# Kernel optimization log

Hardware: AMD Instinct MI355X
Metric: run time of the kernel (lower is better)

The kernel has to match this reference:

```python
import jax, jax.numpy as jnp
import numpy as np

N_ROLES = 6
EPS = 1e-5

def _ln(x, scale, bias):
    m = jnp.mean(x, axis=-1, keepdims=True)
    v = jnp.var(x, axis=-1, keepdims=True)
    return (x - m) * jax.lax.rsqrt(v + EPS) * scale + bias

def setup_inputs() -> dict:
    key = jax.random.key(0)
    ks = jax.random.split(key, 20)
    T, B, D_OBS, H, A = 32, 1024, 256, 512, 32
    inp = {
        'rnn_states': jax.random.normal(ks[0], (B, H), jnp.float32),
        'obs': jax.random.normal(ks[1], (T, B, D_OBS), jnp.float32),
        'resets': jnp.zeros((T, B), jnp.float32),
        'available_actions': jnp.ones((T, B, A), jnp.float32),
        'role_ids': jax.random.randint(ks[2], (T, B), 0, N_ROLES, jnp.int32),
        # feature norm over obs_dim
        'fn_scale': jnp.ones((D_OBS,), jnp.float32),
        'fn_bias': jnp.zeros((D_OBS,), jnp.float32),
        # base MLP: obs_dim->512->512, each followed by LayerNorm
        'W0': jax.random.normal(ks[3], (D_OBS, H), jnp.float32) * 0.02,
        'b0': jnp.zeros((H,), jnp.float32),
        'ln0_scale': jnp.ones((H,), jnp.float32),
        'ln0_bias': jnp.zeros((H,), jnp.float32),
        'W1': jax.random.normal(ks[4], (H, H), jnp.float32) * 0.02,
        'b1': jnp.zeros((H,), jnp.float32),
        'ln1_scale': jnp.ones((H,), jnp.float32),
        'ln1_bias': jnp.zeros((H,), jnp.float32),
        # per-role routes: obs_dim->128->H (stacked over roles)
        'Wr0': jax.random.normal(ks[5], (N_ROLES, D_OBS, 128), jnp.float32) * 0.02,
        'br0': jnp.zeros((N_ROLES, 128), jnp.float32),
        'Wr1': jax.random.normal(ks[6], (N_ROLES, 128, H), jnp.float32) * 0.02,
        'br1': jnp.zeros((N_ROLES, H), jnp.float32),
        # per-role heads: H->64->32->action_dim (stacked over roles)
        'Wh0': jax.random.normal(ks[7], (N_ROLES, H, 64), jnp.float32) * 0.02,
        'bh0': jnp.zeros((N_ROLES, 64), jnp.float32),
        'Wh1': jax.random.normal(ks[8], (N_ROLES, 64, 32), jnp.float32) * 0.02,
        'bh1': jnp.zeros((N_ROLES, 32), jnp.float32),
        'Wh2': jax.random.normal(ks[9], (N_ROLES, 32, A), jnp.float32) * 0.02,
        'bh2': jnp.zeros((N_ROLES, A), jnp.float32),
    }
    return inp

def _gather_by_role(all_values, role_ids):
    # all_values: (K, T, B, F); role_ids: (T, B) -> (T, B, F)
    idx = role_ids[None, :, :, None].astype(jnp.int32)
    return jnp.take_along_axis(all_values, idx, axis=0)[0]

def reference(rnn_states, obs, resets, available_actions, role_ids,
              fn_scale, fn_bias, W0, b0, ln0_scale, ln0_bias,
              W1, b1, ln1_scale, ln1_bias,
              Wr0, br0, Wr1, br1,
              Wh0, bh0, Wh1, bh1, Wh2, bh2):
    # feature normalization on raw obs
    obs_n = _ln(obs, fn_scale, fn_bias)
    # shared base MLP (relu + LayerNorm after each Dense)
    e = _ln(jax.nn.relu(obs_n @ W0 + b0), ln0_scale, ln0_bias)
    e = _ln(jax.nn.relu(e @ W1 + b1), ln1_scale, ln1_bias)
    # per-role pre-GRU residual routes on (normalized) obs
    r = jax.nn.relu(jnp.einsum('tbi,kih->ktbh', obs_n, Wr0) + br0[:, None, None, :])
    r = jax.nn.relu(jnp.einsum('ktbh,kho->ktbo', r, Wr1) + br1[:, None, None, :])
    e = e + _gather_by_role(r, role_ids)
    # no recurrent policy configured: rnn_states pass through
    # per-role heads -> all logits (K, T, B, A)
    h = jax.nn.relu(jnp.einsum('tbh,khf->ktbf', e, Wh0) + bh0[:, None, None, :])
    h = jax.nn.relu(jnp.einsum('ktbf,kfg->ktbg', h, Wh1) + bh1[:, None, None, :])
    all_logits = jnp.einsum('ktbg,kga->ktba', h, Wh2) + bh2[:, None, None, :]
    logits = _gather_by_role(all_logits, role_ids)
    logits = jnp.where(available_actions > 0.5, logits, jnp.full_like(logits, -1e10))
    return rnn_states, logits
```

## Files before the change

### kernel.cpp

```cpp
#include <hip/hip_runtime.h>
#include <stdint.h>

typedef unsigned short u16;
typedef unsigned int u32;

using bf16x8 = __attribute__((ext_vector_type(8))) short;
using f32x4  = __attribute__((ext_vector_type(4))) float;

#define DEVINL __device__ __forceinline__

DEVINL float b2f(u16 u) { return __builtin_bit_cast(float, (u32)u << 16); }
DEVINL u16 f2b(float f) {
  u32 u = __builtin_bit_cast(u32, f);
  u += 0x7FFFu + ((u >> 16) & 1u);
  return (u16)(u >> 16);
}

DEVINL void gll16(const u16* src, u16* dst) {
  __builtin_amdgcn_global_load_lds(
      (const __attribute__((address_space(1))) void*)(uintptr_t)src,
      (__attribute__((address_space(3))) void*)(uintptr_t)dst, 16, 0, 0);
}

#define MFMA __builtin_amdgcn_mfma_f32_16x16x32_bf16
#define NROLE 6

DEVINL void tp_tile(const float* __restrict__ s, u16* __restrict__ d,
                    int R, int C, int bx, int by, int z)
{
  __shared__ u16 tile[32][33];
  const size_t mstride = (size_t)R * C;
  s += (size_t)z * mstride;
  d += (size_t)z * mstride;
  int r0 = bx * 32, c0 = by * 32;
  int tx = threadIdx.x & 31, ty = threadIdx.x >> 5;
#pragma unroll
  for (int i = 0; i < 32; i += 8)
    tile[ty + i][tx] = f2b(s[(size_t)(r0 + ty + i) * C + (c0 + tx)]);
  __syncthreads();
#pragma unroll
  for (int i = 0; i < 32; i += 8)
    d[(size_t)(c0 + ty + i) * R + (r0 + tx)] = tile[tx][ty + i];
}

__global__ __launch_bounds__(256) void mega0(
    const float* W0, const float* W1, const float* Wr0, const float* Wr1, const float* Wh0,
    u16* W0t, u16* W1t, u16* Wr0t, u16* Wr1t, u16* Wh0t,
    const int* __restrict__ rid, int* __restrict__ blkCnt,
    const float* __restrict__ rnn, float* __restrict__ outRnn)
{
  int b = blockIdx.x;
  const int tid = threadIdx.x;
  if (b < 1152) {
    if (b < 128)      {            tp_tile(W0, W0t, 256, 512, b % 8,  b / 8, 0); }
    else if (b < 384) { b -= 128;  tp_tile(W1, W1t, 512, 512, b % 16, b / 16, 0); }
    else if (b < 576) { b -= 384;  int t = b / 8;  tp_tile(Wr0, Wr0t, 256, 128, b % 8,  t % 4,  t / 4); }
    else if (b < 960) { b -= 576;  int t = b / 4;  tp_tile(Wr1, Wr1t, 128, 512, b % 4,  t % 16, t / 16); }
    else              { b -= 960;  int t = b / 16; tp_tile(Wh0, Wh0t, 512, 64,  b % 16, t % 2,  t / 2); }
  } else if (b < 1280) {
    b -= 1152;
    __shared__ int h[NROLE];
    if (tid < NROLE) h[tid] = 0;
    __syncthreads();
    atomicAdd(&h[rid[b * 256 + tid]], 1);
    __syncthreads();
    if (tid < NROLE) blkCnt[b * NROLE + tid] = h[tid];
  } else {
    b -= 1280;
    const float4* src = (const float4*)rnn;
    float4* dst = (float4*)outRnn;
    int base = (b * 256 + tid) * 4;
#pragma unroll
    for (int i = 0; i < 4; ++i) dst[base + i] = src[base + i];
  }
}

__global__ __launch_bounds__(256, 2) void g0f(
    const float* __restrict__ obs, const float* __restrict__ fn_s,
    const float* __restrict__ fn_b, const u16* __restrict__ W0t,
    const float* __restrict__ b0, const float* __restrict__ ln0sc,
    const float* __restrict__ ln0bi, u16* __restrict__ obs_n,
    u16* __restrict__ C,
    const int* __restrict__ rid, const int* __restrict__ blkCnt,
    int* __restrict__ bucket, int* __restrict__ baseArr, int* __restrict__ cntArr)
{
  __shared__ __align__(16) u16 smem[20480];
  const int tid = threadIdx.x;

  if (blockIdx.x >= 512) {
    const int bx = blockIdx.x - 512;
    int* c = (int*)smem;
    int* preArr = c + 768;
    int* scnt   = c + 776;
    int* sbase  = c + 784;
    int* h      = c + 792;
    for (int i = tid; i < 128 * NROLE; i += 256) c[i] = blkCnt[i];
    if (tid < NROLE) h[tid] = 0;
    __syncthreads();
    if (tid < NROLE) {
      int k = tid, run = 0, pre = 0;
      for (int b = 0; b < 128; ++b) { if (b == bx) pre = run; run += c[b * NROLE + k]; }
      scnt[k] = run; preArr[k] = pre;
    }
    __syncthreads();
    if (tid == 0) {
      int r = 0;
      for (int k = 0; k < NROLE; ++k) { sbase[k] = r; r += scnt[k]; }
    }
    __syncthreads();
    if (bx == 0 && tid < NROLE) { baseArr[tid] = sbase[tid]; cntArr[tid] = scnt[tid]; }
    int i = bx * 256 + tid;
    int k = rid[i];
    int pos = atomicAdd(&h[k], 1);
    bucket[sbase[k] + preArr[k] + pos] = i;
    return;
  }

  u16* smA     = smem;
  float* redS  = (float*)&smem[16384];
  float* redSS = (float*)&smem[16896];
  float* prm   = (float*)&smem[17408];
  const int rowBase = blockIdx.x * 64;
  const int lane = tid & 63, wave = tid >> 6;
  const int quad = lane >> 4, lm = lane & 15, l7 = lm & 7;

#pragma unroll
  for (int i = tid; i < 512; i += 256) {
    prm[i] = b0[i]; prm[512 + i] = ln0sc[i]; prm[1024 + i] = ln0bi[i];
  }

  {
    const int r = tid >> 2, q = tid & 3;
    const float* xr = obs + (size_t)(rowBase + r) * 256 + q * 64;
    float x[64];
#pragma unroll
    for (int jj = 0; jj < 16; ++jj)
      *(float4*)&x[jj * 4] = *(const float4*)(xr + jj * 4);
    float s = 0.f, s2 = 0.f;
#pragma unroll
    for (int p = 0; p < 64; ++p) { s += x[p]; s2 += x[p] * x[p]; }
    s  += __shfl_xor(s, 1, 64);  s  += __shfl_xor(s, 2, 64);
    s2 += __shfl_xor(s2, 1, 64); s2 += __shfl_xor(s2, 2, 64);
    float m = s * (1.f / 256.f);
    float var = s2 * (1.f / 256.f) - m * m;
    float inv = rsqrtf(var + 1e-5f);
    const float* fs = fn_s + q * 64;
    const float* fb = fn_b + q * 64;
    u16* og = obs_n + (size_t)(rowBase + r) * 256 + q * 64;
#pragma unroll
    for (int j = 0; j < 8; ++j) {
      float4 fs0 = *(const float4*)(fs + j * 8);
      float4 fs1 = *(const float4*)(fs + j * 8 + 4);
      float4 fb0 = *(const float4*)(fb + j * 8);
      float4 fb1 = *(const float4*)(fb + j * 8 + 4);
      u16 yy[8] __attribute__((aligned(16)));
      yy[0] = f2b((x[j*8+0] - m) * inv * fs0.x + fb0.x);
      yy[1] = f2b((x[j*8+1] - m) * inv * fs0.y + fb0.y);
      yy[2] = f2b((x[j*8+2] - m) * inv * fs0.z + fb0.z);
      yy[3] = f2b((x[j*8+3] - m) * inv * fs0.w + fb0.w);
      yy[4] = f2b((x[j*8+4] - m) * inv * fs1.x + fb1.x);
      yy[5] = f2b((x[j*8+5] - m) * inv * fs1.y + fb1.y);
      yy[6] = f2b((x[j*8+6] - m) * inv * fs1.z + fb1.z);
      yy[7] = f2b((x[j*8+7] - m) * inv * fs1.w + fb1.w);
      int cch = q * 8 + j;
      *(uint4*)&smA[r * 256 + ((cch ^ (r & 7)) * 8)] = *(uint4*)yy;
      *(uint4*)(og + j * 8) = *(uint4*)yy;
    }
  }

  const int wn = wave * 128;
  u32 bOff[8];
#pragma unroll
  for (int j = 0; j < 8; ++j)
    bOff[j] = (u32)(wn + j * 16 + lm) * 256u + (u32)(quad * 8);
  f32x4 acc[4][8] = {};
  bf16x8 bR[2][8];
#pragma unroll
  for (int p = 0; p < 2; ++p)
#pragma unroll
    for (int j = 0; j < 8; ++j)
      bR[p][j] = *(const bf16x8*)(W0t + bOff[j] + p * 32);
  __syncthreads();

#pragma unroll
  for (int g = 0; g < 8; ++g) {
    bf16x8 cur[8];
#pragma unroll
    for (int j = 0; j < 8; ++j) cur[j] = bR[g & 1][j];
    if (g + 2 < 8) {
#pragma unroll
      for (int j = 0; j < 8; ++j)
        bR[g & 1][j] = *(const bf16x8*)(W0t + bOff[j] + (g + 2) * 32);
    }
    const int kc = g * 4;
    bf16x8 af[4];
#pragma unroll
    for (int i2 = 0; i2 < 4; ++i2)
      af[i2] = *(const bf16x8*)&smA[(i2 * 16 + lm) * 256 + (((quad + kc) ^ l7) * 8)];
#pragma unroll
    for (int i2 = 0; i2 < 4; ++i2)
#pragma unroll
      for (int j = 0; j < 8; ++j)
        acc[i2][j] = MFMA(af[i2], cur[j], acc[i2][j], 0, 0, 0);
  }

#pragma unroll
  for (int i2 = 0; i2 < 4; ++i2) {
#pragma unroll
    for (int r2 = 0; r2 < 4; ++r2) {
      float s = 0.f, ss = 0.f;
#pragma unroll
      for (int j = 0; j < 8; ++j) {
        float v = fmaxf(acc[i2][j][r2] + prm[wn + j * 16 + lm], 0.f);
        acc[i2][j][r2] = v;
        s += v; ss += v * v;
      }
#pragma unroll
      for (int o = 1; o < 16; o <<= 1) { s += __shfl_xor(s, o, 64); ss += __shfl_xor(ss, o, 64); }
      if (lm == 0) {
        int rowL = i2 * 16 + quad * 4 + r2;
        redS[rowL * 4 + wave] = s;
        redSS[rowL * 4 + wave] = ss;
      }
    }
  }
  __syncthreads();
#pragma unroll
  for (int i2 = 0; i2 < 4; ++i2) {
#pragma unroll
    for (int r2 = 0; r2 < 4; ++r2) {
      int rowL = i2 * 16 + quad * 4 + r2;
      float ts  = redS[rowL * 4 + 0] + redS[rowL * 4 + 1] + redS[rowL * 4 + 2] + redS[rowL * 4 + 3];
      float tss = redSS[rowL * 4 + 0] + redSS[rowL * 4 + 1] + redSS[rowL * 4 + 2] + redSS[rowL * 4 + 3];
      float m = ts * (1.f / 512.f);
      float var = tss * (1.f / 512.f) - m * m;
      float inv = rsqrtf(var + 1e-5f);
      size_t base = (size_t)(rowBase + rowL) * 512;
#pragma unroll
      for (int j = 0; j < 8; ++j) {
        int col = wn + j * 16 + lm;
        float y = (acc[i2][j][r2] - m) * inv * prm[512 + col] + prm[1024 + col];
        C[base + col] = f2b(y);
      }
    }
  }
}

template <int K>
__global__ __launch_bounds__(256, 2) void gemm_ln(
    const u16* __restrict__ A, const u16* __restrict__ Bt,
    const float* __restrict__ bias, const float* __restrict__ lnsc,
    const float* __restrict__ lnbi, u16* __restrict__ C)
{
  constexpr int BK = 128, NI = K / BK, NC = K / 32;
  __shared__ __align__(16) u16 As[2][64 * BK];
  __shared__ float redS[64][4];
  __shared__ float redSS[64][4];
  __shared__ float prm[1536];
  const int tid = threadIdx.x;
  const int rowBase = blockIdx.x * 64;
  const int lane = tid & 63, wave = tid >> 6;
#pragma unroll
  for (int i = tid; i < 512; i += 256) {
    prm[i] = bias[i]; prm[512 + i] = lnsc[i]; prm[1024 + i] = lnbi[i];
  }
  u32 aOff[4];
#pragma unroll
  for (int r = 0; r < 4; ++r) {
    int row = r * 16 + (tid >> 4);
    int chunk = tid & 15;
    aOff[r] = (u32)(rowBase + row) * (u32)K + (u32)((chunk ^ (row & 7)) * 8);
  }
  const int quad = lane >> 4, lm = lane & 15, l7 = lm & 7;
  const int wn = wave * 128;
  u32 bOff[8];
#pragma unroll
  for (int j = 0; j < 8; ++j)
    bOff[j] = (u32)(wn + j * 16 + lm) * (u32)K + (u32)(quad * 8);

  f32x4 acc[4][8] = {};

#pragma unroll
  for (int r = 0; r < 4; ++r)
    gll16(A + aOff[r], &As[0][r * 2048 + wave * 512]);
  bf16x8 bP[8];
#pragma unroll
  for (int j = 0; j < 8; ++j)
    bP[j] = *(const bf16x8*)(Bt + bOff[j]);
  __syncthreads();

  for (int i = 0; i < NI; ++i) {
    const u16* Ab = As[i & 1];
    if (i + 1 < NI) {
#pragma unroll
      for (int r = 0; r < 4; ++r)
        gll16(A + aOff[r] + (i + 1) * BK, &As[(i + 1) & 1][r * 2048 + wave * 512]);
    }
#pragma unroll
    for (int c = 0; c < 4; ++c) {
      const int g = i * 4 + c;
      bf16x8 bN[8];
      if (g + 1 < NC) {
#pragma unroll
        for (int j = 0; j < 8; ++j)
          bN[j] = *(const bf16x8*)(Bt + bOff[j] + (g + 1) * 32);
      }
      const int kc = c * 4;
      bf16x8 af[4];
#pragma unroll
      for (int i2 = 0; i2 < 4; ++i2)
        af[i2] = *(const bf16x8*)&Ab[(i2 * 16 + lm) * BK + (((quad + kc) ^ l7) * 8)];
#pragma unroll
      for (int i2 = 0; i2 < 4; ++i2)
#pragma unroll
        for (int j = 0; j < 8; ++j)
          acc[i2][j] = MFMA(af[i2], bP[j], acc[i2][j], 0, 0, 0);
      if (g + 1 < NC) {
#pragma unroll
        for (int j = 0; j < 8; ++j) bP[j] = bN[j];
      }
    }
    __syncthreads();
  }

#pragma unroll
  for (int i2 = 0; i2 < 4; ++i2) {
#pragma unroll
    for (int r2 = 0; r2 < 4; ++r2) {
      float s = 0.f, ss = 0.f;
#pragma unroll
      for (int j = 0; j < 8; ++j) {
        float v = fmaxf(acc[i2][j][r2] + prm[wn + j * 16 + lm], 0.f);
        acc[i2][j][r2] = v;
        s += v; ss += v * v;
      }
#pragma unroll
      for (int o = 1; o < 16; o <<= 1) { s += __shfl_xor(s, o, 64); ss += __shfl_xor(ss, o, 64); }
      if (lm == 0) {
        int rowL = i2 * 16 + quad * 4 + r2;
        redS[rowL][wave] = s;
        redSS[rowL][wave] = ss;
      }
    }
  }
  __syncthreads();
#pragma unroll
  for (int i2 = 0; i2 < 4; ++i2) {
#pragma unroll
    for (int r2 = 0; r2 < 4; ++r2) {
      int rowL = i2 * 16 + quad * 4 + r2;
      float ts  = redS[rowL][0] + redS[rowL][1] + redS[rowL][2] + redS[rowL][3];
      float tss = redSS[rowL][0] + redSS[rowL][1] + redSS[rowL][2] + redSS[rowL][3];
      float m = ts * (1.f / 512.f);
      float var = tss * (1.f / 512.f) - m * m;
      float inv = rsqrtf(var + 1e-5f);
      size_t base = (size_t)(rowBase + rowL) * 512;
#pragma unroll
      for (int j = 0; j < 8; ++j) {
        int col = wn + j * 16 + lm;
        float y = (acc[i2][j][r2] - m) * inv * prm[512 + col] + prm[1024 + col];
        C[base + col] = f2b(y);
      }
    }
  }
}

__global__ __launch_bounds__(256, 4) void route_head(
    const u16* __restrict__ obs_n, const u16* __restrict__ e,
    const u16* __restrict__ Wr0t, const float* __restrict__ br0,
    const u16* __restrict__ Wr1t, const float* __restrict__ br1,
    const u16* __restrict__ Wh0t, const float* __restrict__ bh0,
    const float* __restrict__ Wh1, const float* __restrict__ bh1,
    const float* __restrict__ Wh2, const float* __restrict__ bh2,
    const float* __restrict__ avail,
    const int* __restrict__ bucket, const int* __restrict__ baseArr,
    const int* __restrict__ cntArr, float* __restrict__ outLogits)
{
  __shared__ __align__(16) u16 sm[20480];
  const int tid = threadIdx.x;

  int cA0, cA1, cA2, cA3, cA4, cA5, bA0, bA1, bA2, bA3, bA4, bA5;
  {
    int4 ca = *(const int4*)cntArr;  int2 cb = *(const int2*)(cntArr + 4);
    int4 ba = *(const int4*)baseArr; int2 bb = *(const int2*)(baseArr + 4);
    cA0 = ca.x; cA1 = ca.y; cA2 = ca.z; cA3 = ca.w; cA4 = cb.x; cA5 = cb.y;
    bA0 = ba.x; bA1 = ba.y; bA2 = ba.z; bA3 = ba.w; bA4 = bb.x; bA5 = bb.y;
  }
  int role = -1, rem = blockIdx.x, cnt = 0, roleBase = 0;
#define TRY_ROLE(k, ck, bk)                                        \
  if (role < 0) {                                                  \
    int tiles = ((ck) + 31) >> 5;                                  \
    if (rem < tiles) { role = (k); cnt = (ck); roleBase = (bk); }  \
    else rem -= tiles;                                             \
  }
  TRY_ROLE(0, cA0, bA0) TRY_ROLE(1, cA1, bA1) TRY_ROLE(2, cA2, bA2)
  TRY_ROLE(3, cA3, bA3) TRY_ROLE(4, cA4, bA4) TRY_ROLE(5, cA5, bA5)
#undef TRY_ROLE
  if (role < 0) return;
  const int limit = cnt;
  const int rowBase = rem * 32;

  const int lane = tid & 63, wave = tid >> 6;
  const int quad = lane >> 4, lm = lane & 15, l7 = lm & 7;

#pragma unroll
  for (int r = 0; r < 8; ++r) {
    int lrow = r * 4 + wave;
    int i = rowBase + lrow;
    if (i >= limit) i = rowBase;
    int grow = bucket[roleBase + i];
    int chunk = tid & 63;
    int sw = (chunk & 56) | ((chunk ^ lrow) & 7);
    gll16(e + (u32)grow * 512u + (u32)(sw * 8), &sm[r * 2048 + wave * 512]);
  }

  int growA0, growA1;
  {
    int i0 = rowBase + lm;        if (i0 >= limit) i0 = rowBase;
    int i1 = rowBase + 16 + lm;   if (i1 >= limit) i1 = rowBase;
    growA0 = bucket[roleBase + i0];
    growA1 = bucket[roleBase + i1];
  }
  const u16* Ag0 = obs_n + (size_t)growA0 * 256;
  const u16* Ag1 = obs_n + (size_t)growA1 * 256;

  const int wn0 = wave * 32;
  const u16* B0 = Wr0t + (size_t)role * 128 * 256;
  f32x4 acc0[2][2] = {};
  bf16x8 b0R[2][2];
#pragma unroll
  for (int p = 0; p < 2; ++p)
#pragma unroll
    for (int j = 0; j < 2; ++j)
      b0R[p][j] = *(const bf16x8*)(B0 + (u32)(wn0 + j * 16 + lm) * 256u + (u32)(quad * 8 + p * 32));
  bf16x8 aR[4][2];
#pragma unroll
  for (int p = 0; p < 4; ++p) {
    aR[p][0] = *(const bf16x8*)(Ag0 + (u32)(quad * 8 + p * 32));
    aR[p][1] = *(const bf16x8*)(Ag1 + (u32)(quad * 8 + p * 32));
  }
  float bias0[2] = { br0[role * 128 + wn0 + lm], br0[role * 128 + wn0 + 16 + lm] };
#pragma unroll
  for (int it = 0; it < 8; ++it) {
    bf16x8 a0 = aR[it & 3][0], a1 = aR[it & 3][1];
    bf16x8 cur0 = b0R[it & 1][0], cur1 = b0R[it & 1][1];
    if (it + 2 < 8) {
#pragma unroll
      for (int j = 0; j < 2; ++j)
        b0R[it & 1][j] = *(const bf16x8*)(B0 + (u32)(wn0 + j * 16 + lm) * 256u + (u32)(quad * 8 + (it + 2) * 32));
    }
    if (it + 4 < 8) {
      aR[it & 3][0] = *(const bf16x8*)(Ag0 + (u32)(quad * 8 + (it + 4) * 32));
      aR[it & 3][1] = *(const bf16x8*)(Ag1 + (u32)(quad * 8 + (it + 4) * 32));
    }
    acc0[0][0] = MFMA(a0, cur0, acc0[0][0], 0, 0, 0);
    acc0[0][1] = MFMA(a0, cur1, acc0[0][1], 0, 0, 0);
    acc0[1][0] = MFMA(a1, cur0, acc0[1][0], 0, 0, 0);
    acc0[1][1] = MFMA(a1, cur1, acc0[1][1], 0, 0, 0);
  }
  u16* r1 = sm + 16384;
#pragma unroll
  for (int i2 = 0; i2 < 2; ++i2) {
#pragma unroll
    for (int r2 = 0; r2 < 4; ++r2) {
      int row = i2 * 16 + quad * 4 + r2;
#pragma unroll
      for (int j = 0; j < 2; ++j) {
        int col = wn0 + j * 16 + lm;
        float v = fmaxf(acc0[i2][j][r2] + bias0[j], 0.f);
        r1[row * 128 + (((col >> 3) ^ (row & 7)) * 8) + (col & 7)] = f2b(v);
      }
    }
  }
  __syncthreads();

  const int wn1 = wave * 128;
  const u16* B1 = Wr1t + (size_t)role * 512 * 128;
#pragma unroll
  for (int h = 0; h < 2; ++h) {
    const int wnh = wn1 + h * 64;
    float b1v[4];
#pragma unroll
    for (int j = 0; j < 4; ++j) b1v[j] = br1[role * 512 + wnh + j * 16 + lm];
    f32x4 acc1[2][4] = {};
    bf16x8 b1P[4];
#pragma unroll
    for (int j = 0; j < 4; ++j)
      b1P[j] = *(const bf16x8*)(B1 + (u32)(wnh + j * 16 + lm) * 128u + (u32)(quad * 8));
#pragma unroll
    for (int kk = 0; kk < 128; kk += 32) {
      bf16x8 b1N[4];
      if (kk + 32 < 128) {
#pragma unroll
        for (int j = 0; j < 4; ++j)
          b1N[j] = *(const bf16x8*)(B1 + (u32)(wnh + j * 16 + lm) * 128u + (u32)(quad * 8 + kk + 32));
      }
      const int kc = kk >> 3;
      bf16x8 af[2];
#pragma unroll
      for (int i2 = 0; i2 < 2; ++i2)
        af[i2] = *(const bf16x8*)&r1[(i2 * 16 + lm) * 128 + (((quad + kc) ^ l7) * 8)];
#pragma unroll
      for (int i2 = 0; i2 < 2; ++i2)
#pragma unroll
        for (int j = 0; j < 4; ++j)
          acc1[i2][j] = MFMA(af[i2], b1P[j], acc1[i2][j], 0, 0, 0);
      if (kk + 32 < 128) {
#pragma unroll
        for (int j = 0; j < 4; ++j) b1P[j] = b1N[j];
      }
    }
#pragma unroll
    for (int i2 = 0; i2 < 2; ++i2) {
#pragma unroll
      for (int r2 = 0; r2 < 4; ++r2) {
        int row = i2 * 16 + quad * 4 + r2;
#pragma unroll
        for (int j = 0; j < 4; ++j) {
          int col = wnh + j * 16 + lm;
          int addr = row * 512 + (((col >> 3) ^ (row & 7)) * 8) + (col & 7);
          float v = fmaxf(acc1[i2][j][r2] + b1v[j], 0.f) + b2f(sm[addr]);
          sm[addr] = f2b(v);
        }
      }
    }
  }
  __syncthreads();

  const int wn2 = wave * 16;
  const u16* B2 = Wh0t + (size_t)role * 64 * 512;
  float b2v = bh0[role * 64 + wn2 + lm];
  f32x4 acc2[2] = {};
  bf16x8 b2R[4];
#pragma unroll
  for (int p = 0; p < 4; ++p)
    b2R[p] = *(const bf16x8*)(B2 + (u32)(wn2 + lm) * 512u + (u32)(quad * 8 + p * 32));
#pragma unroll
  for (int it = 0; it < 16; ++it) {
    bf16x8 cur = b2R[it & 3];
    if (it + 4 < 16)
      b2R[it & 3] = *(const bf16x8*)(B2 + (u32)(wn2 + lm) * 512u + (u32)(quad * 8 + (it + 4) * 32));
    const int kc = it * 4;
    bf16x8 af[2];
#pragma unroll
    for (int i2 = 0; i2 < 2; ++i2)
      af[i2] = *(const bf16x8*)&sm[(i2 * 16 + lm) * 512 + (((quad + kc) ^ l7) * 8)];
#pragma unroll
    for (int i2 = 0; i2 < 2; ++i2)
      acc2[i2] = MFMA(af[i2], cur, acc2[i2], 0, 0, 0);
  }
  u16* h0s = sm + 16384;
#pragma unroll
  for (int i2 = 0; i2 < 2; ++i2) {
#pragma unroll
    for (int r2 = 0; r2 < 4; ++r2) {
      int row = i2 * 16 + quad * 4 + r2;
      int col = wn2 + lm;
      h0s[row * 68 + col] = f2b(fmaxf(acc2[i2][r2] + b2v, 0.f));
    }
  }
  __syncthreads();

  {
    float* h1s = (float*)&sm[16384];
    const int r = tid >> 3;
    const int n0 = (tid & 7) * 4;
    const bool valid = (rowBase + r) < limit;
    const float* W1k = Wh1 + (size_t)role * 64 * 32;
    const float* W2k = Wh2 + (size_t)role * 32 * 32;
    float4 a1 = *(const float4*)(bh1 + role * 32 + n0);
#pragma unroll 8
    for (int j = 0; j < 64; ++j) {
      float hj = b2f(h0s[r * 68 + j]);
      float4 wv = *(const float4*)(W1k + j * 32 + n0);
      a1.x += hj * wv.x; a1.y += hj * wv.y; a1.z += hj * wv.z; a1.w += hj * wv.w;
    }
    a1.x = fmaxf(a1.x, 0.f); a1.y = fmaxf(a1.y, 0.f);
    a1.z = fmaxf(a1.z, 0.f); a1.w = fmaxf(a1.w, 0.f);
    __syncthreads();
    h1s[r * 36 + n0 + 0] = a1.x;
    h1s[r * 36 + n0 + 1] = a1.y;
    h1s[r * 36 + n0 + 2] = a1.z;
    h1s[r * 36 + n0 + 3] = a1.w;
    __syncthreads();
    float4 a2 = *(const float4*)(bh2 + role * 32 + n0);
#pragma unroll 8
    for (int n = 0; n < 32; ++n) {
      float hn = h1s[r * 36 + n];
      float4 wv = *(const float4*)(W2k + n * 32 + n0);
      a2.x += hn * wv.x; a2.y += hn * wv.y; a2.z += hn * wv.z; a2.w += hn * wv.w;
    }
    if (valid) {
      int g = bucket[roleBase + rowBase + r];
      float4 av = *(const float4*)(avail + (size_t)g * 32 + n0);
      float4 o;
      o.x = (av.x > 0.5f) ? a2.x : -1e10f;
      o.y = (av.y > 0.5f) ? a2.y : -1e10f;
      o.z = (av.z > 0.5f) ? a2.z : -1e10f;
      o.w = (av.w > 0.5f) ? a2.w : -1e10f;
      *(float4*)(outLogits + (size_t)g * 32 + n0) = o;
    }
  }
}

extern "C" void kernel_launch(void* const* d_in, const int* in_sizes, int n_in,
                              void* d_out, int out_size, void* d_ws, size_t ws_size,
                              hipStream_t stream)
{
  const float* rnn  = (const float*)d_in[0];
  const float* obs  = (const float*)d_in[1];
  const float* avail= (const float*)d_in[3];
  const int*   rid  = (const int*)d_in[4];
  const float* fn_s = (const float*)d_in[5];
  const float* fn_b = (const float*)d_in[6];
  const float* W0   = (const float*)d_in[7];
  const float* b0   = (const float*)d_in[8];
  const float* ln0s = (const float*)d_in[9];
  const float* ln0b = (const float*)d_in[10];
  const float* W1   = (const float*)d_in[11];
  const float* b1   = (const float*)d_in[12];
  const float* ln1s = (const float*)d_in[13];
  const float* ln1b = (const float*)d_in[14];
  const float* Wr0  = (const float*)d_in[15];
  const float* br0  = (const float*)d_in[16];
  const float* Wr1  = (const float*)d_in[17];
  const float* br1  = (const float*)d_in[18];
  const float* Wh0  = (const float*)d_in[19];
  const float* bh0  = (const float*)d_in[20];
  const float* Wh1  = (const float*)d_in[21];
  const float* bh1  = (const float*)d_in[22];
  const float* Wh2  = (const float*)d_in[23];
  const float* bh2  = (const float*)d_in[24];

  const int ROWS = 32768;

  char* w = (char*)d_ws;
  auto carve = [&](size_t bytes) { char* p = w; w += (bytes + 255) & ~(size_t)255; return p; };
  u16* obs_n  = (u16*)carve((size_t)ROWS * 256 * 2);
  u16* bufA   = (u16*)carve((size_t)ROWS * 512 * 2);
  u16* bufB   = (u16*)carve((size_t)ROWS * 512 * 2);
  u16* W0t    = (u16*)carve((size_t)512 * 256 * 2);
  u16* W1t    = (u16*)carve((size_t)512 * 512 * 2);
  u16* Wr0t   = (u16*)carve((size_t)6 * 128 * 256 * 2);
  u16* Wr1t   = (u16*)carve((size_t)6 * 512 * 128 * 2);
  u16* Wh0t   = (u16*)carve((size_t)6 * 64 * 512 * 2);
  int* bucket = (int*)carve((size_t)ROWS * 4);
  int* blkCnt = (int*)carve((size_t)128 * NROLE * 4);
  int* baseArr= (int*)carve(256);
  int* cntArr = (int*)carve(256);

  float* outLogits = (float*)d_out + (size_t)1024 * 512;

  mega0<<<1408, 256, 0, stream>>>(W0, W1, Wr0, Wr1, Wh0, W0t, W1t, Wr0t, Wr1t, Wh0t,
                                  rid, blkCnt, rnn, (float*)d_out);

  g0f<<<640, 256, 0, stream>>>(obs, fn_s, fn_b, W0t, b0, ln0s, ln0b,
                               obs_n, bufA, rid, blkCnt, bucket, baseArr, cntArr);

  gemm_ln<512><<<512, 256, 0, stream>>>(bufA, W1t, b1, ln1s, ln1b, bufB);

  route_head<<<1029, 256, 0, stream>>>(obs_n, bufB, Wr0t, br0, Wr1t, br1, Wh0t, bh0,
                                       Wh1, bh1, Wh2, bh2, avail,
                                       bucket, baseArr, cntArr, outLogits);
}
```

Baseline: 271.1 us.

## Restructure route_head as single-wave blocks over 16-row tiles without barriers

The route/head kernel now runs one 64-thread wave per block on 16-row tiles instead of four waves on 32-row tiles, with 2053 blocks instead of 1029. Each wave computes every output column itself, which removes all __syncthreads and shrinks shared memory per block. The intent is more independent blocks, less barrier stalling and higher occupancy. The cost is that each wave reloads the full per-role weight tiles from global or cache with no software prefetch, and the tail MLP now handles 8 columns per lane.

```diff
diff --git a/kernel.cpp b/kernel.cpp
--- a/kernel.cpp
+++ b/kernel.cpp
@@ -365,7 +365,7 @@
   }
 }
 
-__global__ __launch_bounds__(256, 4) void route_head(
+__global__ __launch_bounds__(64, 2) void route_head(
     const u16* __restrict__ obs_n, const u16* __restrict__ e,
     const u16* __restrict__ Wr0t, const float* __restrict__ br0,
     const u16* __restrict__ Wr1t, const float* __restrict__ br1,
@@ -376,8 +376,8 @@
     const int* __restrict__ bucket, const int* __restrict__ baseArr,
     const int* __restrict__ cntArr, float* __restrict__ outLogits)
 {
-  __shared__ __align__(16) u16 sm[20480];
-  const int tid = threadIdx.x;
+  __shared__ __align__(16) u16 sm[11328];
+  const int lane = threadIdx.x;
 
   int cA0, cA1, cA2, cA3, cA4, cA5, bA0, bA1, bA2, bA3, bA4, bA5;
   {
@@ -389,7 +389,7 @@
   int role = -1, rem = blockIdx.x, cnt = 0, roleBase = 0;
 #define TRY_ROLE(k, ck, bk)                                        \
   if (role < 0) {                                                  \
-    int tiles = ((ck) + 31) >> 5;                                  \
+    int tiles = ((ck) + 15) >> 4;                                  \
     if (rem < tiles) { role = (k); cnt = (ck); roleBase = (bk); }  \
     else rem -= tiles;                                             \
   }
@@ -398,207 +398,148 @@
 #undef TRY_ROLE
   if (role < 0) return;
   const int limit = cnt;
-  const int rowBase = rem * 32;
-
-  const int lane = tid & 63, wave = tid >> 6;
-  const int quad = lane >> 4, lm = lane & 15, l7 = lm & 7;
-
-#pragma unroll
-  for (int r = 0; r < 8; ++r) {
-    int lrow = r * 4 + wave;
+  const int rowBase = rem * 16;
+
+  const int quad = lane >> 4, lm = lane & 15;
+
+#pragma unroll
+  for (int lrow = 0; lrow < 16; ++lrow) {
     int i = rowBase + lrow;
     if (i >= limit) i = rowBase;
     int grow = bucket[roleBase + i];
-    int chunk = tid & 63;
-    int sw = (chunk & 56) | ((chunk ^ lrow) & 7);
-    gll16(e + (u32)grow * 512u + (u32)(sw * 8), &sm[r * 2048 + wave * 512]);
-  }
-
-  int growA0, growA1;
+    int sw = (lane & 56) | ((lane ^ lrow) & 7);
+    gll16(e + (u32)grow * 512u + (u32)(sw * 8), &sm[lrow * 512]);
+  }
+
+  int iA = rowBase + lm; if (iA >= limit) iA = rowBase;
+  const u16* Ag = obs_n + (size_t)bucket[roleBase + iA] * 256 + quad * 8;
+
+  const u16* B0 = Wr0t + (size_t)role * 128 * 256;
+  f32x4 acc0[8] = {};
+#pragma unroll
+  for (int kc = 0; kc < 8; ++kc) {
+    bf16x8 a = *(const bf16x8*)(Ag + kc * 32);
+#pragma unroll
+    for (int j = 0; j < 8; ++j) {
+      bf16x8 b = *(const bf16x8*)(B0 + (u32)(j * 16 + lm) * 256u + (u32)(kc * 32 + quad * 8));
+      acc0[j] = MFMA(a, b, acc0[j], 0, 0, 0);
+    }
+  }
+  u16* r1 = sm + 8192;
+#pragma unroll
+  for (int j = 0; j < 8; ++j) {
+    float bv = br0[role * 128 + j * 16 + lm];
+#pragma unroll
+    for (int r2 = 0; r2 < 4; ++r2) {
+      int row = quad * 4 + r2;
+      int col = j * 16 + lm;
+      float v = fmaxf(acc0[j][r2] + bv, 0.f);
+      r1[row * 128 + (((col >> 3) ^ (row & 7)) * 8) + (col & 7)] = f2b(v);
+    }
+  }
+
+  const u16* B1 = Wr1t + (size_t)role * 512 * 128;
+#pragma unroll
+  for (int g = 0; g < 4; ++g) {
+    f32x4 acc1[8] = {};
+#pragma unroll
+    for (int kc = 0; kc < 4; ++kc) {
+      bf16x8 a = *(const bf16x8*)&r1[lm * 128 + (((kc * 4 + quad) ^ (lm & 7)) * 8)];
+#pragma unroll
+      for (int j = 0; j < 8; ++j) {
+        int col = g * 128 + j * 16 + lm;
+        bf16x8 b = *(const bf16x8*)(B1 + (u32)col * 128u + (u32)(kc * 32 + quad * 8));
+        acc1[j] = MFMA(a, b, acc1[j], 0, 0, 0);
+      }
+    }
+    if (g == 0) {
+      asm volatile("s_waitcnt vmcnt(0)" ::: "memory");
+      __builtin_amdgcn_sched_barrier(0);
+    }
+#pragma unroll
+    for (int j = 0; j < 8; ++j) {
+      int col = g * 128 + j * 16 + lm;
+      float bv = br1[role * 512 + col];
+#pragma unroll
+      for (int r2 = 0; r2 < 4; ++r2) {
+        int row = quad * 4 + r2;
+        int addr = row * 512 + (((col >> 3) ^ (row & 7)) * 8) + (col & 7);
+        float v = fmaxf(acc1[j][r2] + bv, 0.f) + b2f(sm[addr]);
+        sm[addr] = f2b(v);
+      }
+    }
+  }
+
+  const u16* B2 = Wh0t + (size_t)role * 64 * 512;
+  f32x4 acc2[4] = {};
+#pragma unroll
+  for (int kt = 0; kt < 16; ++kt) {
+    bf16x8 a = *(const bf16x8*)&sm[lm * 512 + (((kt * 4 + quad) ^ (lm & 7)) * 8)];
+#pragma unroll
+    for (int j = 0; j < 4; ++j) {
+      bf16x8 b = *(const bf16x8*)(B2 + (u32)(j * 16 + lm) * 512u + (u32)(kt * 32 + quad * 8));
+      acc2[j] = MFMA(a, b, acc2[j], 0, 0, 0);
+    }
+  }
+  u16* h0s = sm + 10240;
+#pragma unroll
+  for (int j = 0; j < 4; ++j) {
+    float bv = bh0[role * 64 + j * 16 + lm];
+#pragma unroll
+    for (int r2 = 0; r2 < 4; ++r2) {
+      int row = quad * 4 + r2;
+      h0s[row * 68 + j * 16 + lm] = f2b(fmaxf(acc2[j][r2] + bv, 0.f));
+    }
+  }
+
   {
-    int i0 = rowBase + lm;        if (i0 >= limit) i0 = rowBase;
-    int i1 = rowBase + 16 + lm;   if (i1 >= limit) i1 = rowBase;
-    growA0 = bucket[roleBase + i0];
-    growA1 = bucket[roleBase + i1];
-  }
-  const u16* Ag0 = obs_n + (size_t)growA0 * 256;
-  const u16* Ag1 = obs_n + (size_t)growA1 * 256;
-
-  const int wn0 = wave * 32;
-  const u16* B0 = Wr0t + (size_t)role * 128 * 256;
-  f32x4 acc0[2][2] = {};
-  bf16x8 b0R[2][2];
-#pragma unroll
-  for (int p = 0; p < 2; ++p)
-#pragma unroll
-    for (int j = 0; j < 2; ++j)
-      b0R[p][j] = *(const bf16x8*)(B0 + (u32)(wn0 + j * 16 + lm) * 256u + (u32)(quad * 8 + p * 32));
-  bf16x8 aR[4][2];
-#pragma unroll
-  for (int p = 0; p < 4; ++p) {
-    aR[p][0] = *(const bf16x8*)(Ag0 + (u32)(quad * 8 + p * 32));
-    aR[p][1] = *(const bf16x8*)(Ag1 + (u32)(quad * 8 + p * 32));
-  }
-  float bias0[2] = { br0[role * 128 + wn0 + lm], br0[role * 128 + wn0 + 16 + lm] };
-#pragma unroll
-  for (int it = 0; it < 8; ++it) {
-    bf16x8 a0 = aR[it & 3][0], a1 = aR[it & 3][1];
-    bf16x8 cur0 = b0R[it & 1][0], cur1 = b0R[it & 1][1];
-    if (it + 2 < 8) {
-#pragma unroll
-      for (int j = 0; j < 2; ++j)
-        b0R[it & 1][j] = *(const bf16x8*)(B0 + (u32)(wn0 + j * 16 + lm) * 256u + (u32)(quad * 8 + (it + 2) * 32));
-    }
-    if (it + 4 < 8) {
-      aR[it & 3][0] = *(const bf16x8*)(Ag0 + (u32)(quad * 8 + (it + 4) * 32));
-      aR[it & 3][1] = *(const bf16x8*)(Ag1 + (u32)(quad * 8 + (it + 4) * 32));
-    }
-    acc0[0][0] = MFMA(a0, cur0, acc0[0][0], 0, 0, 0);
-    acc0[0][1] = MFMA(a0, cur1, acc0[0][1], 0, 0, 0);
-    acc0[1][0] = MFMA(a1, cur0, acc0[1][0], 0, 0, 0);
-    acc0[1][1] = MFMA(a1, cur1, acc0[1][1], 0, 0, 0);
-  }
-  u16* r1 = sm + 16384;
-#pragma unroll
-  for (int i2 = 0; i2 < 2; ++i2) {
-#pragma unroll
-    for (int r2 = 0; r2 < 4; ++r2) {
-      int row = i2 * 16 + quad * 4 + r2;
-#pragma unroll
-      for (int j = 0; j < 2; ++j) {
-        int col = wn0 + j * 16 + lm;
-        float v = fmaxf(acc0[i2][j][r2] + bias0[j], 0.f);
-        r1[row * 128 + (((col >> 3) ^ (row & 7)) * 8) + (col & 7)] = f2b(v);
-      }
-    }
-  }
-  __syncthreads();
-
-  const int wn1 = wave * 128;
-  const u16* B1 = Wr1t + (size_t)role * 512 * 128;
-#pragma unroll
-  for (int h = 0; h < 2; ++h) {
-    const int wnh = wn1 + h * 64;
-    float b1v[4];
-#pragma unroll
-    for (int j = 0; j < 4; ++j) b1v[j] = br1[role * 512 + wnh + j * 16 + lm];
-    f32x4 acc1[2][4] = {};
-    bf16x8 b1P[4];
-#pragma unroll
-    for (int j = 0; j < 4; ++j)
-      b1P[j] = *(const bf16x8*)(B1 + (u32)(wnh + j * 16 + lm) * 128u + (u32)(quad * 8));
-#pragma unroll
-    for (int kk = 0; kk < 128; kk += 32) {
-      bf16x8 b1N[4];
-      if (kk + 32 < 128) {
-#pragma unroll
-        for (int j = 0; j < 4; ++j)
-          b1N[j] = *(const bf16x8*)(B1 + (u32)(wnh + j * 16 + lm) * 128u + (u32)(quad * 8 + kk + 32));
-      }
-      const int kc = kk >> 3;
-      bf16x8 af[2];
-#pragma unroll
-      for (int i2 = 0; i2 < 2; ++i2)
-        af[i2] = *(const bf16x8*)&r1[(i2 * 16 + lm) * 128 + (((quad + kc) ^ l7) * 8)];
-#pragma unroll
-      for (int i2 = 0; i2 < 2; ++i2)
-#pragma unroll
-        for (int j = 0; j < 4; ++j)
-          acc1[i2][j] = MFMA(af[i2], b1P[j], acc1[i2][j], 0, 0, 0);
-      if (kk + 32 < 128) {
-#pragma unroll
-        for (int j = 0; j < 4; ++j) b1P[j] = b1N[j];
-      }
-    }
-#pragma unroll
-    for (int i2 = 0; i2 < 2; ++i2) {
-#pragma unroll
-      for (int r2 = 0; r2 < 4; ++r2) {
-        int row = i2 * 16 + quad * 4 + r2;
-#pragma unroll
-        for (int j = 0; j < 4; ++j) {
-          int col = wnh + j * 16 + lm;
-          int addr = row * 512 + (((col >> 3) ^ (row & 7)) * 8) + (col & 7);
-          float v = fmaxf(acc1[i2][j][r2] + b1v[j], 0.f) + b2f(sm[addr]);
-          sm[addr] = f2b(v);
-        }
-      }
-    }
-  }
-  __syncthreads();
-
-  const int wn2 = wave * 16;
-  const u16* B2 = Wh0t + (size_t)role * 64 * 512;
-  float b2v = bh0[role * 64 + wn2 + lm];
-  f32x4 acc2[2] = {};
-  bf16x8 b2R[4];
-#pragma unroll
-  for (int p = 0; p < 4; ++p)
-    b2R[p] = *(const bf16x8*)(B2 + (u32)(wn2 + lm) * 512u + (u32)(quad * 8 + p * 32));
-#pragma unroll
-  for (int it = 0; it < 16; ++it) {
-    bf16x8 cur = b2R[it & 3];
-    if (it + 4 < 16)
-      b2R[it & 3] = *(const bf16x8*)(B2 + (u32)(wn2 + lm) * 512u + (u32)(quad * 8 + (it + 4) * 32));
-    const int kc = it * 4;
-    bf16x8 af[2];
-#pragma unroll
-    for (int i2 = 0; i2 < 2; ++i2)
-      af[i2] = *(const bf16x8*)&sm[(i2 * 16 + lm) * 512 + (((quad + kc) ^ l7) * 8)];
-#pragma unroll
-    for (int i2 = 0; i2 < 2; ++i2)
-      acc2[i2] = MFMA(af[i2], cur, acc2[i2], 0, 0, 0);
-  }
-  u16* h0s = sm + 16384;
-#pragma unroll
-  for (int i2 = 0; i2 < 2; ++i2) {
-#pragma unroll
-    for (int r2 = 0; r2 < 4; ++r2) {
-      int row = i2 * 16 + quad * 4 + r2;
-      int col = wn2 + lm;
-      h0s[row * 68 + col] = f2b(fmaxf(acc2[i2][r2] + b2v, 0.f));
-    }
-  }
-  __syncthreads();
-
-  {
-    float* h1s = (float*)&sm[16384];
-    const int r = tid >> 3;
-    const int n0 = (tid & 7) * 4;
+    float* h1s = (float*)&sm[8192];
+    const int r = lane >> 2;
+    const int n0 = (lane & 3) * 8;
     const bool valid = (rowBase + r) < limit;
     const float* W1k = Wh1 + (size_t)role * 64 * 32;
     const float* W2k = Wh2 + (size_t)role * 32 * 32;
-    float4 a1 = *(const float4*)(bh1 + role * 32 + n0);
+    float4 a1a = *(const float4*)(bh1 + role * 32 + n0);
+    float4 a1b = *(const float4*)(bh1 + role * 32 + n0 + 4);
 #pragma unroll 8
     for (int j = 0; j < 64; ++j) {
       float hj = b2f(h0s[r * 68 + j]);
-      float4 wv = *(const float4*)(W1k + j * 32 + n0);
-      a1.x += hj * wv.x; a1.y += hj * wv.y; a1.z += hj * wv.z; a1.w += hj * wv.w;
-    }
-    a1.x = fmaxf(a1.x, 0.f); a1.y = fmaxf(a1.y, 0.f);
-    a1.z = fmaxf(a1.z, 0.f); a1.w = fmaxf(a1.w, 0.f);
-    __syncthreads();
-    h1s[r * 36 + n0 + 0] = a1.x;
-    h1s[r * 36 + n0 + 1] = a1.y;
-    h1s[r * 36 + n0 + 2] = a1.z;
-    h1s[r * 36 + n0 + 3] = a1.w;
-    __syncthreads();
-    float4 a2 = *(const float4*)(bh2 + role * 32 + n0);
+      float4 wa = *(const float4*)(W1k + j * 32 + n0);
+      float4 wb = *(const float4*)(W1k + j * 32 + n0 + 4);
+      a1a.x += hj * wa.x; a1a.y += hj * wa.y; a1a.z += hj * wa.z; a1a.w += hj * wa.w;
+      a1b.x += hj * wb.x; a1b.y += hj * wb.y; a1b.z += hj * wb.z; a1b.w += hj * wb.w;
+    }
+    a1a.x = fmaxf(a1a.x, 0.f); a1a.y = fmaxf(a1a.y, 0.f);
+    a1a.z = fmaxf(a1a.z, 0.f); a1a.w = fmaxf(a1a.w, 0.f);
+    a1b.x = fmaxf(a1b.x, 0.f); a1b.y = fmaxf(a1b.y, 0.f);
+    a1b.z = fmaxf(a1b.z, 0.f); a1b.w = fmaxf(a1b.w, 0.f);
+    *(float4*)(h1s + r * 36 + n0)     = a1a;
+    *(float4*)(h1s + r * 36 + n0 + 4) = a1b;
+    float4 a2a = *(const float4*)(bh2 + role * 32 + n0);
+    float4 a2b = *(const float4*)(bh2 + role * 32 + n0 + 4);
 #pragma unroll 8
     for (int n = 0; n < 32; ++n) {
       float hn = h1s[r * 36 + n];
-      float4 wv = *(const float4*)(W2k + n * 32 + n0);
-      a2.x += hn * wv.x; a2.y += hn * wv.y; a2.z += hn * wv.z; a2.w += hn * wv.w;
+      float4 wa = *(const float4*)(W2k + n * 32 + n0);
+      float4 wb = *(const float4*)(W2k + n * 32 + n0 + 4);
+      a2a.x += hn * wa.x; a2a.y += hn * wa.y; a2a.z += hn * wa.z; a2a.w += hn * wa.w;
+      a2b.x += hn * wb.x; a2b.y += hn * wb.y; a2b.z += hn * wb.z; a2b.w += hn * wb.w;
     }
     if (valid) {
       int g = bucket[roleBase + rowBase + r];
-      float4 av = *(const float4*)(avail + (size_t)g * 32 + n0);
-      float4 o;
-      o.x = (av.x > 0.5f) ? a2.x : -1e10f;
-      o.y = (av.y > 0.5f) ? a2.y : -1e10f;
-      o.z = (av.z > 0.5f) ? a2.z : -1e10f;
-      o.w = (av.w > 0.5f) ? a2.w : -1e10f;
-      *(float4*)(outLogits + (size_t)g * 32 + n0) = o;
+      float4 ava = *(const float4*)(avail + (size_t)g * 32 + n0);
+      float4 avb = *(const float4*)(avail + (size_t)g * 32 + n0 + 4);
+      float4 oa, ob;
+      oa.x = (ava.x > 0.5f) ? a2a.x : -1e10f;
+      oa.y = (ava.y > 0.5f) ? a2a.y : -1e10f;
+      oa.z = (ava.z > 0.5f) ? a2a.z : -1e10f;
+      oa.w = (ava.w > 0.5f) ? a2a.w : -1e10f;
+      ob.x = (avb.x > 0.5f) ? a2b.x : -1e10f;
+      ob.y = (avb.y > 0.5f) ? a2b.y : -1e10f;
+      ob.z = (avb.z > 0.5f) ? a2b.z : -1e10f;
+      ob.w = (avb.w > 0.5f) ? a2b.w : -1e10f;
+      *(float4*)(outLogits + (size_t)g * 32 + n0)     = oa;
+      *(float4*)(outLogits + (size_t)g * 32 + n0 + 4) = ob;
     }
   }
 }
@@ -659,7 +600,7 @@
 
   gemm_ln<512><<<512, 256, 0, stream>>>(bufA, W1t, b1, ln1s, ln1b, bufB);
 
-  route_head<<<1029, 256, 0, stream>>>(obs_n, bufB, Wr0t, br0, Wr1t, br1, Wh0t, bh0,
-                                       Wh1, bh1, Wh2, bh2, avail,
-                                       bucket, baseArr, cntArr, outLogits);
-}
+  route_head<<<2053, 64, 0, stream>>>(obs_n, bufB, Wr0t, br0, Wr1t, br1, Wh0t, bh0,
+                                      Wh1, bh1, Wh2, bh2, avail,
+                                      bucket, baseArr, cntArr, outLogits);
+}
```

Result: slower. 311.9 us (+15.1%).
